# Optimization experiments

Hardware: AMD Instinct MI355X
Metric: run time of the kernel (lower is better)

Reference implementation:

```python
import jax, jax.numpy as jnp
import numpy as np

BLOCK = 64      # InformationEntropyAnalyzer block_size
BINS = 256      # InformationEntropyAnalyzer num_bins
EPS = 1e-12


def setup_inputs() -> dict:
    key = jax.random.key(0)
    x = jax.random.normal(key, (8, 64, 256, 256), dtype=jnp.float32)
    return {"x": x}


def _block_entropy(blocks):
    """Shannon entropy per block, matching np.histogram(density=True) math.

    blocks: (B, n) float32. Returns (B,) float32.
    """
    B, n = blocks.shape
    bmin = jnp.min(blocks, axis=1, keepdims=True)            # (B,1)
    bmax = jnp.max(blocks, axis=1, keepdims=True)            # (B,1)
    width = (bmax - bmin) / BINS                              # uniform bin width
    width_safe = jnp.where(width > 0, width, 1.0)
    # np.histogram: rightmost edge inclusive -> floor + clip reproduces it
    idx = jnp.clip(jnp.floor((blocks - bmin) / width_safe), 0, BINS - 1).astype(jnp.int32)
    row = jnp.arange(B, dtype=jnp.int32)[:, None]
    flat = (row * BINS + idx).reshape(-1)
    counts = jax.ops.segment_sum(
        jnp.ones((B * n,), jnp.float32), flat, num_segments=B * BINS
    ).reshape(B, BINS)
    density = counts / (n * width_safe)                       # density=True normalization
    p = density + EPS
    p = p / jnp.sum(p, axis=1, keepdims=True)
    return -jnp.sum(p * jnp.log2(p), axis=1)


def reference(x):
    """Faithful JAX version of InformationEntropyAnalyzer._compute_4d_entropy.

    Per (n,c) slice: split HxW into BLOCKxBLOCK tiles, compute Shannon entropy
    of the 256-bin histogram of each tile, then bilinearly upsample
    (align_corners=False, i.e. half-pixel, = jax.image.resize 'linear')
    back to (H, W).  Output: (N, C, H, W) entropy map.
    """
    N, C, H, W = x.shape
    nbh, nbw = H // BLOCK, W // BLOCK  # evenly divisible by construction
    blocks = (
        x.reshape(N, C, nbh, BLOCK, nbw, BLOCK)
        .transpose(0, 1, 2, 4, 3, 5)
        .reshape(N * C * nbh * nbw, BLOCK * BLOCK)
    )
    ent = _block_entropy(blocks).reshape(N, C, nbh, nbw)
    # F.interpolate(mode='bilinear', align_corners=False) == half-pixel linear resize
    return jax.image.resize(ent, (N, C, H, W), method='linear')
```

## Files before the change

kernel.cpp:

```cpp
#include <hip/hip_runtime.h>

#define NBINS 256
#define EPSF 1e-12f

typedef float v4f __attribute__((ext_vector_type(4)));

__global__ __launch_bounds__(256, 2) void fused_kernel(const float* __restrict__ x,
                                                       float* __restrict__ out) {
    const int nc   = blockIdx.x;
    const int t    = threadIdx.x;
    const int lane = t & 63;
    const int wave = t >> 6;

    __shared__ unsigned int hist[4][NBINS];
    __shared__ float ent_s[16];

    const float* rbase = x + ((size_t)nc << 16) + (size_t)wave * (64 * 256);
    unsigned int* h = hist[wave];

    v4f va[16], vb[16];

#define ISSUE(buf, col)                                                           \
    _Pragma("unroll")                                                             \
    for (int k = 0; k < 16; ++k) {                                                \
        const int f = lane + (k << 6);                    \
        buf[k] = *reinterpret_cast<const v4f*>(                                   \
            rbase + (col) * 64 + (size_t)(f >> 4) * 256 + (f & 15) * 4);          \
    }

#define PROCESS(buf, col)                                                         \
    {                                                                             \
        float lmin = INFINITY, lmax = -INFINITY;                                  \
        _Pragma("unroll")                                                         \
        for (int k = 0; k < 16; ++k) {                                            \
            lmin = fminf(lmin, fminf(fminf(buf[k].x, buf[k].y),                   \
                                     fminf(buf[k].z, buf[k].w)));                 \
            lmax = fmaxf(lmax, fmaxf(fmaxf(buf[k].x, buf[k].y),                   \
                                     fmaxf(buf[k].z, buf[k].w)));                 \
        }                                                                         \
        _Pragma("unroll")                                                         \
        for (int off = 32; off > 0; off >>= 1) {                                  \
            lmin = fminf(lmin, __shfl_xor(lmin, off));                            \
            lmax = fmaxf(lmax, __shfl_xor(lmax, off));                            \
        }                                                                         \
        uint4 z; z.x = z.y = z.z = z.w = 0u;       \
        reinterpret_cast<uint4*>(h)[lane] = z;                                    \
        const float width = (lmax - lmin) * (1.0f / NBINS);                       \
        const float wsafe = (width > 0.0f) ? width : 1.0f;                        \
        const float inv   = 1.0f / wsafe;                                         \
        const float coff  = -lmin * inv;                                          \
        _Pragma("unroll")                                                         \
        for (int k = 0; k < 16; ++k) {                                            \
            float vals[4] = {buf[k].x, buf[k].y, buf[k].z, buf[k].w};             \
            _Pragma("unroll")                                                     \
            for (int j = 0; j < 4; ++j) {                                         \
                      \
                int bin = (int)fmaf(vals[j], inv, coff);                          \
                bin = min(bin, 255);                                              \
                atomicAdd(&h[bin], 1u);                                           \
            }                                                                     \
        }                                                                         \
        const uint4 c    = reinterpret_cast<const uint4*>(h)[lane];               \
        const float pden = inv * (1.0f / 4096.0f);            \
        const float p0 = (float)c.x * pden + EPSF;                                \
        const float p1 = (float)c.y * pden + EPSF;                                \
        const float p2 = (float)c.z * pden + EPSF;                                \
        const float p3 = (float)c.w * pden + EPSF;                                \
        float s = p0 + p1 + p2 + p3;                                              \
        _Pragma("unroll")                                                         \
        for (int off = 32; off > 0; off >>= 1) s += __shfl_xor(s, off);           \
        const float itot = 1.0f / s;                                              \
        const float q0 = p0 * itot, q1 = p1 * itot;                               \
        const float q2 = p2 * itot, q3 = p3 * itot;                               \
        float e = q0 * log2f(q0) + q1 * log2f(q1)                                 \
                + q2 * log2f(q2) + q3 * log2f(q3);                                \
        _Pragma("unroll")                                                         \
        for (int off = 32; off > 0; off >>= 1) e += __shfl_xor(e, off);           \
        if (lane == 0) ent_s[(wave << 2) + (col)] = -e;                           \
    }

    ISSUE(va, 0)
    ISSUE(vb, 1)
    PROCESS(va, 0)
    ISSUE(va, 2)
    PROCESS(vb, 1)
    ISSUE(vb, 3)
    PROCESS(va, 2)
    PROCESS(vb, 3)
#undef ISSUE
#undef PROCESS

    __syncthreads();

    const int x4 = t & 63;
    const int yy = wave;

    const int ix = (int)floorf(((x4 << 2) + 0.5f) * 0.015625f - 0.5f);
    const int x0 = max(ix, 0), x1 = min(ix + 1, 3);
    v4f wv[4];
#pragma unroll
    for (int j = 0; j < 4; ++j) {
        const float fx = ((x4 << 2) + j + 0.5f) * 0.015625f - 0.5f;
        const float wx = fx - floorf(fx);
        const float a  = 1.0f - wx, bb = wx;
        wv[j].x = ((x0 == 0) ? a : 0.0f) + ((x1 == 0) ? bb : 0.0f);
        wv[j].y = ((x0 == 1) ? a : 0.0f) + ((x1 == 1) ? bb : 0.0f);
        wv[j].z = ((x0 == 2) ? a : 0.0f) + ((x1 == 2) ? bb : 0.0f);
        wv[j].w = ((x0 == 3) ? a : 0.0f) + ((x1 == 3) ? bb : 0.0f);
    }

    const v4f* er = reinterpret_cast<const v4f*>(ent_s);
    v4f* out4 = reinterpret_cast<v4f*>(out) + ((size_t)nc << 14);
#pragma unroll 8
    for (int it = 0; it < 64; ++it) {
        const int   y   = (it << 2) + yy;
        const float fy  = (y + 0.5f) * 0.015625f - 0.5f;
        const float fiy = floorf(fy);
        const float wy  = fy - fiy;
        const int   iy  = (int)fiy;
        const int   y0  = max(iy, 0), y1 = min(iy + 1, 3);
        const float wy0 = 1.0f - wy;

        const v4f r0 = er[y0];
        const v4f r1 = er[y1];
        v4f rv = r0 * wy0 + r1 * wy;
        v4f o;
        o.x = rv.x * wv[0].x + rv.y * wv[0].y + rv.z * wv[0].z + rv.w * wv[0].w;
        o.y = rv.x * wv[1].x + rv.y * wv[1].y + rv.z * wv[1].z + rv.w * wv[1].w;
        o.z = rv.x * wv[2].x + rv.y * wv[2].y + rv.z * wv[2].z + rv.w * wv[2].w;
        o.w = rv.x * wv[3].x + rv.y * wv[3].y + rv.z * wv[3].z + rv.w * wv[3].w;
        out4[(y << 6) + x4] = o;
    }
}

extern "C" void kernel_launch(void* const* d_in, const int* in_sizes, int n_in,
                              void* d_out, int out_size, void* d_ws, size_t ws_size,
                              hipStream_t stream) {
    const float* x   = (const float*)d_in[0];
    float*       out = (float*)d_out;
    fused_kernel<<<512, 256, 0, stream>>>(x, out);
}
```

Measured before the change: 45.25 us.

## Process blocks row-by-row and interleave output writes with entropy compute

Each of the 4 waves now handles one block column, and the four waves sweep the block rows in sequence instead of each wave taking one block row. Once the entropy values needed for a quarter of the output are ready, a barrier is hit and that quarter is upsampled and stored while later block rows are still being processed. The aim is to overlap the large output write stream with histogram compute instead of doing all the stores at the end. The cost is extra barriers and heavier instruction interleaving, which may raise register pressure.

```diff
diff --git a/kernel.cpp b/kernel.cpp
--- a/kernel.cpp
+++ b/kernel.cpp
@@ -15,20 +15,20 @@
     __shared__ unsigned int hist[4][NBINS];
     __shared__ float ent_s[16];
 
-    const float* rbase = x + ((size_t)nc << 16) + (size_t)wave * (64 * 256);
+    const float* cbase = x + ((size_t)nc << 16) + (size_t)wave * 64;
     unsigned int* h = hist[wave];
 
     v4f va[16], vb[16];
 
-#define ISSUE(buf, col)                                                           \
+#define ISSUE(buf, s)                                                             \
     _Pragma("unroll")                                                             \
     for (int k = 0; k < 16; ++k) {                                                \
         const int f = lane + (k << 6);                    \
         buf[k] = *reinterpret_cast<const v4f*>(                                   \
-            rbase + (col) * 64 + (size_t)(f >> 4) * 256 + (f & 15) * 4);          \
+            cbase + (size_t)(s) * (64 * 256) + (size_t)(f >> 4) * 256 + (f & 15) * 4); \
     }
 
-#define PROCESS(buf, col)                                                         \
+#define PROCESS(buf, s)                                                           \
     {                                                                             \
         float lmin = INFINITY, lmax = -INFINITY;                                  \
         _Pragma("unroll")                                                         \
@@ -66,35 +66,20 @@
         const float p1 = (float)c.y * pden + EPSF;                                \
         const float p2 = (float)c.z * pden + EPSF;                                \
         const float p3 = (float)c.w * pden + EPSF;                                \
-        float s = p0 + p1 + p2 + p3;                                              \
+        float s_ = p0 + p1 + p2 + p3;                                             \
         _Pragma("unroll")                                                         \
-        for (int off = 32; off > 0; off >>= 1) s += __shfl_xor(s, off);           \
-        const float itot = 1.0f / s;                                              \
+        for (int off = 32; off > 0; off >>= 1) s_ += __shfl_xor(s_, off);         \
+        const float itot = 1.0f / s_;                                             \
         const float q0 = p0 * itot, q1 = p1 * itot;                               \
         const float q2 = p2 * itot, q3 = p3 * itot;                               \
         float e = q0 * log2f(q0) + q1 * log2f(q1)                                 \
                 + q2 * log2f(q2) + q3 * log2f(q3);                                \
         _Pragma("unroll")                                                         \
         for (int off = 32; off > 0; off >>= 1) e += __shfl_xor(e, off);           \
-        if (lane == 0) ent_s[(wave << 2) + (col)] = -e;                           \
+        if (lane == 0) ent_s[((s) << 2) + wave] = -e;                             \
     }
 
-    ISSUE(va, 0)
-    ISSUE(vb, 1)
-    PROCESS(va, 0)
-    ISSUE(va, 2)
-    PROCESS(vb, 1)
-    ISSUE(vb, 3)
-    PROCESS(va, 2)
-    PROCESS(vb, 3)
-#undef ISSUE
-#undef PROCESS
-
-    __syncthreads();
-
-    const int x4 = t & 63;
-    const int yy = wave;
-
+    const int x4 = lane;
     const int ix = (int)floorf(((x4 << 2) + 0.5f) * 0.015625f - 0.5f);
     const int x0 = max(ix, 0), x1 = min(ix + 1, 3);
     v4f wv[4];
@@ -108,29 +93,48 @@
         wv[j].z = ((x0 == 2) ? a : 0.0f) + ((x1 == 2) ? bb : 0.0f);
         wv[j].w = ((x0 == 3) ? a : 0.0f) + ((x1 == 3) ? bb : 0.0f);
     }
-
     const v4f* er = reinterpret_cast<const v4f*>(ent_s);
     v4f* out4 = reinterpret_cast<v4f*>(out) + ((size_t)nc << 14);
-#pragma unroll 8
-    for (int it = 0; it < 64; ++it) {
-        const int   y   = (it << 2) + yy;
-        const float fy  = (y + 0.5f) * 0.015625f - 0.5f;
-        const float fiy = floorf(fy);
-        const float wy  = fy - fiy;
-        const int   iy  = (int)fiy;
-        const int   y0  = max(iy, 0), y1 = min(iy + 1, 3);
-        const float wy0 = 1.0f - wy;
 
-        const v4f r0 = er[y0];
-        const v4f r1 = er[y1];
-        v4f rv = r0 * wy0 + r1 * wy;
-        v4f o;
-        o.x = rv.x * wv[0].x + rv.y * wv[0].y + rv.z * wv[0].z + rv.w * wv[0].w;
-        o.y = rv.x * wv[1].x + rv.y * wv[1].y + rv.z * wv[1].z + rv.w * wv[1].w;
-        o.z = rv.x * wv[2].x + rv.y * wv[2].y + rv.z * wv[2].z + rv.w * wv[2].w;
-        o.w = rv.x * wv[3].x + rv.y * wv[3].y + rv.z * wv[3].z + rv.w * wv[3].w;
-        out4[(y << 6) + x4] = o;
+#define WQ(q)                                                                     \
+    _Pragma("unroll")                                                             \
+    for (int i = 0; i < 16; ++i) {                                                \
+        const int   y   = ((q) << 6) + (wave << 4) + i;                           \
+        const float fy  = (y + 0.5f) * 0.015625f - 0.5f;                          \
+        const float fiy = floorf(fy);                                             \
+        const float wy  = fy - fiy;                                               \
+        const int   iy  = (int)fiy;                                               \
+        const int   y0  = max(iy, 0), y1 = min(iy + 1, 3);                        \
+        const v4f r0 = er[y0];                 \
+        const v4f r1 = er[y1];                                                    \
+        v4f rv = r0 * (1.0f - wy) + r1 * wy;                                      \
+        v4f o;                                                                    \
+        o.x = rv.x * wv[0].x + rv.y * wv[0].y + rv.z * wv[0].z + rv.w * wv[0].w;  \
+        o.y = rv.x * wv[1].x + rv.y * wv[1].y + rv.z * wv[1].z + rv.w * wv[1].w;  \
+        o.z = rv.x * wv[2].x + rv.y * wv[2].y + rv.z * wv[2].z + rv.w * wv[2].w;  \
+        o.w = rv.x * wv[3].x + rv.y * wv[3].y + rv.z * wv[3].z + rv.w * wv[3].w;  \
+        out4[(y << 6) + x4] = o;                                                  \
     }
+
+    ISSUE(va, 0)
+    ISSUE(vb, 1)
+    PROCESS(va, 0)
+    ISSUE(va, 2)
+    PROCESS(vb, 1)
+    ISSUE(vb, 3)
+    __syncthreads();
+    WQ(0)
+    PROCESS(va, 2)
+    __syncthreads();
+    WQ(1)
+    PROCESS(vb, 3)
+    __syncthreads();
+    WQ(2)
+    WQ(3)
+
+#undef ISSUE
+#undef PROCESS
+#undef WQ
 }
 
 extern "C" void kernel_launch(void* const* d_in, const int* in_sizes, int n_in,
```

Result: faster. 43.44 us (-4.0%).
